# Performance work log

Hardware: AMD Instinct MI355X
Metric: run time of the kernel (lower is better)

The kernel has to match this reference:

```python
import jax, jax.numpy as jnp
import numpy as np

G = 7          # 7x7 feature map -> 49 nodes per image
N = G * G
K = 3          # knn_k
NEG_SLOPE = 0.2  # PyG GATConv default leaky_relu slope


def build_spatial_edges():
    # 8-neighborhood grid edges on the 7x7 map, directed (src -> dst)
    src, dst = [], []
    for r in range(G):
        for c in range(G):
            i = r * G + c
            for dr in (-1, 0, 1):
                for dc in (-1, 0, 1):
                    if dr == 0 and dc == 0:
                        continue
                    rr, cc = r + dr, c + dc
                    if 0 <= rr < G and 0 <= cc < G:
                        src.append(rr * G + cc)
                        dst.append(i)
    return np.array([src, dst], dtype=np.int32)

SPATIAL = build_spatial_edges()  # [2, 312]


def build_edges(x):
    """x: [B, N, F] node features -> (src, dst) each [B, E].
    Edges = spatial 8-neighborhood + feature-space kNN (k=3) + self-loops."""
    B = x.shape[0]
    sq = jnp.sum(x * x, axis=-1)                               # [B, N]
    d = sq[:, :, None] + sq[:, None, :] - 2.0 * jnp.einsum('bnf,bmf->bnm', x, x)
    d = d + jnp.eye(N, dtype=x.dtype) * 1e9                    # exclude self
    _, nbr = jax.lax.top_k(-d, K)                              # [B, N, K]
    knn_src = nbr.reshape(B, N * K)
    knn_dst = jnp.broadcast_to(jnp.repeat(jnp.arange(N, dtype=jnp.int32), K)[None], (B, N * K))
    sp = jnp.asarray(SPATIAL)
    Es = sp.shape[1]
    loops = jnp.arange(N, dtype=jnp.int32)
    src = jnp.concatenate([jnp.broadcast_to(sp[0][None], (B, Es)), knn_src.astype(jnp.int32),
                           jnp.broadcast_to(loops[None], (B, N))], axis=1)
    dst = jnp.concatenate([jnp.broadcast_to(sp[1][None], (B, Es)), knn_dst,
                           jnp.broadcast_to(loops[None], (B, N))], axis=1)
    return src, dst


def gat_layer(x, src, dst, W, a_src, a_dst, b, concat):
    """PyG-style GATConv (eval mode, no dropout). x: [N,F], src/dst: [E]."""
    H, C = a_src.shape
    h = (x @ W).reshape(N, H, C)                               # [N, H, C]
    es = jnp.sum(h * a_src[None], axis=-1)                     # [N, H]
    ed = jnp.sum(h * a_dst[None], axis=-1)                     # [N, H]
    e = jax.nn.leaky_relu(es[src] + ed[dst], NEG_SLOPE)        # [E, H]
    m = jax.ops.segment_max(e, dst, num_segments=N)            # [N, H]
    m = jnp.where(jnp.isfinite(m), m, 0.0)
    p = jnp.exp(e - m[dst])
    denom = jax.ops.segment_sum(p, dst, num_segments=N)
    alpha = p / jnp.maximum(denom[dst], 1e-16)                 # softmax over incoming edges
    out = jax.ops.segment_sum(alpha[:, :, None] * h[src], dst, num_segments=N)  # [N, H, C]
    out = out.reshape(N, H * C) if concat else out.mean(axis=1)
    return out + b


def setup_inputs() -> dict:
    key = jax.random.key(0)
    ks = jax.random.split(key, 14)
    B, F, Hd, Cd, O, NC = 256, 1024, 8, 128, 256, 14
    s = 0.05
    return {
        'feat_map': jax.random.normal(ks[0], (B, F, G, G), dtype=jnp.float32),
        'W1': jax.random.normal(ks[1], (F, Hd * Cd), dtype=jnp.float32) * s,
        'a_src1': jax.random.normal(ks[2], (Hd, Cd), dtype=jnp.float32) * s,
        'a_dst1': jax.random.normal(ks[3], (Hd, Cd), dtype=jnp.float32) * s,
        'b1': jnp.zeros((Hd * Cd,), dtype=jnp.float32),
        'W2': jax.random.normal(ks[4], (Hd * Cd, O), dtype=jnp.float32) * s,
        'a_src2': jax.random.normal(ks[5], (1, O), dtype=jnp.float32) * s,
        'a_dst2': jax.random.normal(ks[6], (1, O), dtype=jnp.float32) * s,
        'b2': jnp.zeros((O,), dtype=jnp.float32),
        'Wc1': jax.random.normal(ks[7], (O, O), dtype=jnp.float32) * s,
        'bc1': jnp.zeros((O,), dtype=jnp.float32),
        'Wc2': jax.random.normal(ks[8], (O, NC), dtype=jnp.float32) * s,
        'bc2': jnp.zeros((NC,), dtype=jnp.float32),
    }


def reference(feat_map, W1, a_src1, a_dst1, b1, W2, a_src2, a_dst2, b2, Wc1, bc1, Wc2, bc2):
    B = feat_map.shape[0]
    # backbone output relu + flatten 7x7 map into 49 nodes
    x = jax.nn.relu(feat_map).reshape(B, -1, N).transpose(0, 2, 1)  # [B, N, 1024]
    src, dst = build_edges(x)

    def per_graph(xg, sg, dg):
        h = jax.nn.elu(gat_layer(xg, sg, dg, W1, a_src1, a_dst1, b1, True))
        h = jax.nn.elu(gat_layer(h, sg, dg, W2, a_src2, a_dst2, b2, False))
        return h.mean(axis=0)                                   # global mean pool -> [256]

    pooled = jax.vmap(per_graph)(x, src, dst)                   # [B, 256]
    return jax.nn.relu(pooled @ Wc1 + bc1) @ Wc2 + bc2          # [B, 14]
```

## Files before the change

### kernel.cpp

```cpp
#include <hip/hip_runtime.h>

#define GDIM 7
#define NN 49
#define FDIM 1024
#define HD 8
#define CD 128
#define ODIM 256
#define NC 14
#define MAXE 12
#define KSPLIT 4
#define GPSTRIDE 3192

typedef __attribute__((ext_vector_type(4))) float f32x4;
typedef __attribute__((ext_vector_type(8))) short s16x8;

struct us4 { unsigned short x, y, z, w; };

__device__ __forceinline__ unsigned short f2bf(float x) {
  unsigned u = __float_as_uint(x);
  return (unsigned short)((u + 0x7fffu + ((u >> 16) & 1u)) >> 16);
}
__device__ __forceinline__ float bf2f(unsigned short h) {
  return __uint_as_float((unsigned)h << 16);
}

#define GLOAD_LDS16(g, l)                                          \
  __builtin_amdgcn_global_load_lds(                                \
      (const __attribute__((address_space(1))) void*)(g),          \
      (__attribute__((address_space(3))) void*)(l), 16, 0, 0)

__global__ void __launch_bounds__(256) relu_transpose_kernel(
    const float* __restrict__ F, float* __restrict__ X,
    unsigned short* __restrict__ Xh, unsigned short* __restrict__ Xl) {
  const int b  = blockIdx.x >> 4;
  const int f0 = (blockIdx.x & 15) << 6;
  const int tid = threadIdx.x;
  __shared__ float lds[64 * NN];
  const float* src = F + (size_t)b * FDIM * NN + (size_t)f0 * NN;
  for (int idx = tid; idx < 64 * NN; idx += 256) lds[idx] = src[idx];
  __syncthreads();
  for (int pass = 0; pass < 13; pass++) {
    int n = pass * 4 + (tid >> 6);
    int fi = tid & 63;
    if (n < NN) {
      float v = lds[fi * NN + n];
      v = v > 0.f ? v : 0.f;
      size_t o = ((size_t)b * NN + n) * FDIM + f0 + fi;
      X[o] = v;
      unsigned short h = f2bf(v);
      Xh[o] = h;
      Xl[o] = f2bf(v - bf2f(h));
    }
  }
}

__global__ void __launch_bounds__(256) knn_partial(
    const float* __restrict__ X, float* __restrict__ gramP) {
  const int gid = blockIdx.x;
  const int b = gid >> 2, p = gid & 3;
  const int tid = threadIdx.x;
  __shared__ float xs[56][68];
  const float* Xb = X + (size_t)b * NN * FDIM + p * 256;

  const int tr = tid / 14, tc = tid % 14;
  float acc[4][4];
#pragma unroll
  for (int i = 0; i < 4; i++)
#pragma unroll
    for (int j = 0; j < 4; j++) acc[i][j] = 0.f;

  for (int c0 = 0; c0 < 256; c0 += 64) {
    __syncthreads();
    for (int idx = tid; idx < NN * 16; idx += 256) {
      int n = idx >> 4, q = idx & 15;
      *(float4*)&xs[n][q << 2] =
          *(const float4*)&Xb[(size_t)n * FDIM + c0 + (q << 2)];
    }
    __syncthreads();
    if (tid < 196) {
#pragma unroll
      for (int k4 = 0; k4 < 64; k4 += 4) {
        float4 a[4], bb[4];
#pragma unroll
        for (int i = 0; i < 4; i++) a[i]  = *(const float4*)&xs[tr + 14 * i][k4];
#pragma unroll
        for (int j = 0; j < 4; j++) bb[j] = *(const float4*)&xs[tc + 14 * j][k4];
#pragma unroll
        for (int i = 0; i < 4; i++)
#pragma unroll
          for (int j = 0; j < 4; j++)
            acc[i][j] += a[i].x * bb[j].x + a[i].y * bb[j].y +
                         a[i].z * bb[j].z + a[i].w * bb[j].w;
      }
    }
  }
  if (tid < 196) {
    float* gp = gramP + (size_t)gid * GPSTRIDE;
#pragma unroll
    for (int i = 0; i < 4; i++)
#pragma unroll
      for (int j = 0; j < 4; j++)
        gp[(tr + 14 * i) * 57 + tc + 14 * j] = acc[i][j];
  }
}

__global__ void __launch_bounds__(256) knn_select(
    const float* __restrict__ gramP, int* __restrict__ knn) {
  const int b = blockIdx.x, tid = threadIdx.x;
  __shared__ float gram[NN][50];
  const float* g0 = gramP + (size_t)(b * KSPLIT) * GPSTRIDE;
  for (int idx = tid; idx < NN * NN; idx += 256) {
    int r = idx / NN, c = idx % NN;
    float s = g0[r * 57 + c] + g0[GPSTRIDE + r * 57 + c] +
              g0[2 * GPSTRIDE + r * 57 + c] + g0[3 * GPSTRIDE + r * 57 + c];
    gram[r][c] = s;
  }
  __syncthreads();
  if (tid < NN) {
    const int n = tid;
    const float sqn = gram[n][n];
    float d0 = 1e30f, d1 = 1e30f, d2 = 1e30f;
    int i0 = 0, i1 = 0, i2 = 0;
    for (int m = 0; m < NN; m++) {
      if (m == n) continue;
      float d = sqn + gram[m][m] - 2.f * gram[n][m];
      if (d < d0)      { d2=d1; i2=i1; d1=d0; i1=i0; d0=d; i0=m; }
      else if (d < d1) { d2=d1; i2=i1; d1=d;  i1=m; }
      else if (d < d2) { d2=d;  i2=m; }
    }
    knn[((size_t)b * NN + n) * 3 + 0] = i0;
    knn[((size_t)b * NN + n) * 3 + 1] = i1;
    knn[((size_t)b * NN + n) * 3 + 2] = i2;
  }
}

__global__ void __launch_bounds__(256) wconvT_kernel(
    const float* __restrict__ W, int K, int N,
    unsigned short* __restrict__ WhT, unsigned short* __restrict__ WlT) {
  __shared__ float t[64][65];
  const int nbx = N >> 6;
  const int bx = blockIdx.x % nbx, by = blockIdx.x / nbx;
  const int r0 = by << 6, c0 = bx << 6;
  const int tid = threadIdx.x;
#pragma unroll
  for (int i = 0; i < 16; i++) {
    int r = i * 4 + (tid >> 6), c = tid & 63;
    t[r][c] = W[(size_t)(r0 + r) * N + c0 + c];
  }
  __syncthreads();
#pragma unroll
  for (int i = 0; i < 16; i++) {
    int n = i * 4 + (tid >> 6);
    int k = tid & 63;
    float x = t[k][n];
    unsigned short h = f2bf(x);
    size_t o = (size_t)(c0 + n) * K + r0 + k;
    WhT[o] = h;
    WlT[o] = f2bf(x - bf2f(h));
  }
}

__global__ void __launch_bounds__(256) gemm_bf16x3(
    const unsigned short* __restrict__ A_h, const unsigned short* __restrict__ A_l,
    const unsigned short* __restrict__ BT_h, const unsigned short* __restrict__ BT_l,
    float* __restrict__ C, int M, int N, int K) {
  __shared__ unsigned short sAh[128][64], sAl[128][64];
  __shared__ unsigned short sBh[128][64], sBl[128][64];
  const int tid = threadIdx.x;
  const int w = tid >> 6, lane = tid & 63;
  const int nbx = N >> 7;
  const int nwg = gridDim.x;
  const int q = nwg >> 3, r = nwg & 7;
  const int xcd = blockIdx.x & 7, loc = blockIdx.x >> 3;
  const int wg = (xcd < r) ? (xcd * (q + 1) + loc)
                           : (r * (q + 1) + (xcd - r) * q + loc);
  const int bx = wg % nbx, by = wg / nbx;
  const int row0 = by << 7, col0 = bx << 7;
  const int wr = (w >> 1) << 6, wc = (w & 1) << 6;
  const int sgr = lane >> 3;
  const int schunk = lane & 7;
  const int fr = lane & 15;
  const int fq = lane >> 4;

  f32x4 acc[4][4];
#pragma unroll
  for (int m = 0; m < 4; m++)
#pragma unroll
    for (int n = 0; n < 4; n++) acc[m][n] = (f32x4){0.f, 0.f, 0.f, 0.f};

  for (int k0 = 0; k0 < K; k0 += 64) {
    __syncthreads();
#pragma unroll
    for (int i = 0; i < 4; i++) {
      const int rbase = (w << 5) + (i << 3);
      const int gr = rbase + sgr;
      const int sc = schunk ^ (gr & 7);
      const size_t ga = (size_t)(row0 + gr) * K + k0 + (sc << 3);
      GLOAD_LDS16(A_h + ga, &sAh[rbase][0]);
      GLOAD_LDS16(A_l + ga, &sAl[rbase][0]);
      const size_t gb = (size_t)(col0 + gr) * K + k0 + (sc << 3);
      GLOAD_LDS16(BT_h + gb, &sBh[rbase][0]);
      GLOAD_LDS16(BT_l + gb, &sBl[rbase][0]);
    }
    __syncthreads();
#pragma unroll
    for (int ks = 0; ks < 2; ks++) {
      const int cb = (ks << 2) + fq;
      s16x8 ah[4], al[4], bh[4], bl[4];
#pragma unroll
      for (int m = 0; m < 4; m++) {
        const int ra = wr + (m << 4) + fr;
        const int ca = (cb ^ (ra & 7)) << 3;
        ah[m] = *(const s16x8*)&sAh[ra][ca];
        al[m] = *(const s16x8*)&sAl[ra][ca];
        const int rb = wc + (m << 4) + fr;
        const int cbn = (cb ^ (rb & 7)) << 3;
        bh[m] = *(const s16x8*)&sBh[rb][cbn];
        bl[m] = *(const s16x8*)&sBl[rb][cbn];
      }
#pragma unroll
      for (int m = 0; m < 4; m++)
#pragma unroll
        for (int n = 0; n < 4; n++) {
          acc[m][n] = __builtin_amdgcn_mfma_f32_16x16x32_bf16(ah[m], bh[n], acc[m][n], 0, 0, 0);
          acc[m][n] = __builtin_amdgcn_mfma_f32_16x16x32_bf16(ah[m], bl[n], acc[m][n], 0, 0, 0);
          acc[m][n] = __builtin_amdgcn_mfma_f32_16x16x32_bf16(al[m], bh[n], acc[m][n], 0, 0, 0);
        }
    }
  }
  const int crow = fq << 2, ccol = fr;
#pragma unroll
  for (int m = 0; m < 4; m++)
#pragma unroll
    for (int n = 0; n < 4; n++)
#pragma unroll
      for (int v = 0; v < 4; v++)
        C[(size_t)(row0 + wr + (m << 4) + crow + v) * N + col0 + wc + (n << 4) + ccol] =
            acc[m][n][v];
}

__global__ void __launch_bounds__(256) esed1_kernel(
    const float* __restrict__ H, const float* __restrict__ a_src,
    const float* __restrict__ a_dst, float* __restrict__ es_g,
    float* __restrict__ ed_g) {
  const int n = blockIdx.x * 4 + (threadIdx.x >> 6);
  const int lane = threadIdx.x & 63;
  const int h = lane >> 3, sub = lane & 7;
  const float* hr = H + (size_t)n * FDIM + h * CD + sub * 16;
  const float* as = a_src + h * CD + sub * 16;
  const float* ad = a_dst + h * CD + sub * 16;
  float s1 = 0.f, s2 = 0.f;
#pragma unroll
  for (int c = 0; c < 16; c += 4) {
    float4 hv = *(const float4*)&hr[c];
    float4 av = *(const float4*)&as[c];
    float4 dv = *(const float4*)&ad[c];
    s1 += hv.x*av.x + hv.y*av.y + hv.z*av.z + hv.w*av.w;
    s2 += hv.x*dv.x + hv.y*dv.y + hv.z*dv.z + hv.w*dv.w;
  }
  s1 += __shfl_xor(s1, 1); s1 += __shfl_xor(s1, 2); s1 += __shfl_xor(s1, 4);
  s2 += __shfl_xor(s2, 1); s2 += __shfl_xor(s2, 2); s2 += __shfl_xor(s2, 4);
  if (sub == 0) {
    es_g[(size_t)n * HD + h] = s1;
    ed_g[(size_t)n * HD + h] = s2;
  }
}

__global__ void __launch_bounds__(256) attn1_soft(
    const float* __restrict__ es_g, const float* __restrict__ ed_g,
    const int* __restrict__ knn, int* __restrict__ srcs_g,
    int* __restrict__ cnt_g, float* __restrict__ alpha_g) {
  const int b = blockIdx.x, tid = threadIdx.x;
  __shared__ float es[NN][HD], ed[NN][HD];
  __shared__ int srcs[NN][MAXE];
  __shared__ int cnt[NN];
  for (int p = tid; p < NN * HD; p += 256) {
    es[p >> 3][p & 7] = es_g[(size_t)b * NN * HD + p];
    ed[p >> 3][p & 7] = ed_g[(size_t)b * NN * HD + p];
  }
  if (tid < NN) {
    int i = tid, r = i / GDIM, c = i % GDIM, k = 0;
    for (int dr = -1; dr <= 1; dr++)
      for (int dc = -1; dc <= 1; dc++) {
        if (dr == 0 && dc == 0) continue;
        int rr = r + dr, cc = c + dc;
        if (rr >= 0 && rr < GDIM && cc >= 0 && cc < GDIM)
          srcs[i][k++] = rr * GDIM + cc;
      }
    srcs[i][k++] = knn[((size_t)b * NN + i) * 3 + 0];
    srcs[i][k++] = knn[((size_t)b * NN + i) * 3 + 1];
    srcs[i][k++] = knn[((size_t)b * NN + i) * 3 + 2];
    srcs[i][k++] = i;
    cnt[i] = k;
    cnt_g[(size_t)b * NN + i] = k;
    for (int j = 0; j < MAXE; j++)
      srcs_g[((size_t)b * NN + i) * MAXE + j] = srcs[i][j < k ? j : 0];
  }
  __syncthreads();
  for (int p = tid; p < NN * HD; p += 256) {
    int i = p >> 3, h = p & 7;
    int k = cnt[i];
    float e[MAXE];
    float m = -1e30f;
#pragma unroll
    for (int j = 0; j < MAXE; j++) {
      if (j < k) {
        float v = es[srcs[i][j]][h] + ed[i][h];
        v = v >= 0.f ? v : 0.2f * v;
        e[j] = v;
        m = fmaxf(m, v);
      }
    }
    float denom = 0.f;
#pragma unroll
    for (int j = 0; j < MAXE; j++) {
      if (j < k) { e[j] = expf(e[j] - m); denom += e[j]; }
    }
    float inv = 1.f / fmaxf(denom, 1e-16f);
#pragma unroll
    for (int j = 0; j < MAXE; j++) {
      if (j < k)
        alpha_g[(((size_t)b * NN + i) * MAXE + j) * HD + h] = e[j] * inv;
    }
  }
}

__global__ void __launch_bounds__(256) attn1_agg(
    const float* __restrict__ H, const int* __restrict__ srcs_g,
    const int* __restrict__ cnt_g, const float* __restrict__ alpha_g,
    const float* __restrict__ b1,
    unsigned short* __restrict__ Zh, unsigned short* __restrict__ Zl) {
  const int bid = blockIdx.x;
  const int b = bid / NN;
  const int tid = threadIdx.x;
  __shared__ float al[MAXE][HD];
  __shared__ int ss[MAXE];
  const int k = cnt_g[bid];
  if (tid < MAXE * HD) al[tid >> 3][tid & 7] = alpha_g[(size_t)bid * MAXE * HD + tid];
  if (tid < MAXE) ss[tid] = srcs_g[(size_t)bid * MAXE + tid];
  __syncthreads();
  const float4* Hb = (const float4*)(H + (size_t)b * NN * FDIM);
  const int h = tid >> 5;
  float4 acc = ((const float4*)b1)[tid];
  for (int j = 0; j < k; j++) {
    float a = al[j][h];
    float4 v = Hb[(size_t)ss[j] * (FDIM / 4) + tid];
    acc.x += a * v.x; acc.y += a * v.y; acc.z += a * v.z; acc.w += a * v.w;
  }
  acc.x = acc.x > 0.f ? acc.x : expm1f(acc.x);
  acc.y = acc.y > 0.f ? acc.y : expm1f(acc.y);
  acc.z = acc.z > 0.f ? acc.z : expm1f(acc.z);
  acc.w = acc.w > 0.f ? acc.w : expm1f(acc.w);
  us4 hv, lv;
  hv.x = f2bf(acc.x); lv.x = f2bf(acc.x - bf2f(hv.x));
  hv.y = f2bf(acc.y); lv.y = f2bf(acc.y - bf2f(hv.y));
  hv.z = f2bf(acc.z); lv.z = f2bf(acc.z - bf2f(hv.z));
  hv.w = f2bf(acc.w); lv.w = f2bf(acc.w - bf2f(hv.w));
  *(us4*)&Zh[(size_t)bid * FDIM + (tid << 2)] = hv;
  *(us4*)&Zl[(size_t)bid * FDIM + (tid << 2)] = lv;
}

__global__ void __launch_bounds__(256) esed2_kernel(
    const float* __restrict__ H2, const float* __restrict__ a_src,
    const float* __restrict__ a_dst, float* __restrict__ es_g,
    float* __restrict__ ed_g) {
  const int n = blockIdx.x * 4 + (threadIdx.x >> 6);
  const int lane = threadIdx.x & 63;
  float4 hv = *(const float4*)&H2[(size_t)n * ODIM + lane * 4];
  float4 av = *(const float4*)&a_src[lane * 4];
  float4 dv = *(const float4*)&a_dst[lane * 4];
  float s1 = hv.x*av.x + hv.y*av.y + hv.z*av.z + hv.w*av.w;
  float s2 = hv.x*dv.x + hv.y*dv.y + hv.z*dv.z + hv.w*dv.w;
#pragma unroll
  for (int m = 1; m < 64; m <<= 1) {
    s1 += __shfl_xor(s1, m);
    s2 += __shfl_xor(s2, m);
  }
  if (lane == 0) { es_g[n] = s1; ed_g[n] = s2; }
}

__global__ void __launch_bounds__(256) attn2_soft(
    const float* __restrict__ es_g, const float* __restrict__ ed_g,
    const int* __restrict__ srcs_g, const int* __restrict__ cnt_g,
    float* __restrict__ alpha_g) {
  const int b = blockIdx.x, tid = threadIdx.x;
  __shared__ float es[NN], ed[NN];
  if (tid < NN) {
    es[tid] = es_g[(size_t)b * NN + tid];
    ed[tid] = ed_g[(size_t)b * NN + tid];
  }
  __syncthreads();
  if (tid < NN) {
    const int i = tid;
    const int k = cnt_g[(size_t)b * NN + i];
    float e[MAXE];
    float m = -1e30f;
#pragma unroll
    for (int j = 0; j < MAXE; j++) {
      if (j < k) {
        int s = srcs_g[((size_t)b * NN + i) * MAXE + j];
        float v = es[s] + ed[i];
        v = v >= 0.f ? v : 0.2f * v;
        e[j] = v;
        m = fmaxf(m, v);
      }
    }
    float denom = 0.f;
#pragma unroll
    for (int j = 0; j < MAXE; j++) {
      if (j < k) { e[j] = expf(e[j] - m); denom += e[j]; }
    }
    float inv = 1.f / fmaxf(denom, 1e-16f);
#pragma unroll
    for (int j = 0; j < MAXE; j++) {
      if (j < k) alpha_g[((size_t)b * NN + i) * MAXE + j] = e[j] * inv;
    }
  }
}

__global__ void __launch_bounds__(256) attn2_agg(
    const float* __restrict__ H2, const int* __restrict__ srcs_g,
    const int* __restrict__ cnt_g, const float* __restrict__ alpha_g,
    const float* __restrict__ b2, float* __restrict__ Z2) {
  const int bid = blockIdx.x;
  const int b = bid / NN;
  const int tid = threadIdx.x;
  __shared__ float al[MAXE];
  __shared__ int ss[MAXE];
  const int k = cnt_g[bid];
  if (tid < MAXE) {
    al[tid] = alpha_g[(size_t)bid * MAXE + tid];
    ss[tid] = srcs_g[(size_t)bid * MAXE + tid];
  }
  __syncthreads();
  const float* Hb = H2 + (size_t)b * NN * ODIM;
  float acc = b2[tid];
  for (int j = 0; j < k; j++)
    acc += al[j] * Hb[(size_t)ss[j] * ODIM + tid];
  acc = acc > 0.f ? acc : expm1f(acc);
  Z2[(size_t)bid * ODIM + tid] = acc;
}

__global__ void __launch_bounds__(256) classifier_kernel(
    const float* __restrict__ Z2, const float* __restrict__ Wc1,
    const float* __restrict__ bc1, const float* __restrict__ Wc2,
    const float* __restrict__ bc2, float* __restrict__ out) {
  const int b = blockIdx.x, tid = threadIdx.x;
  __shared__ float p[ODIM];
  __shared__ float t[ODIM];
  float s = 0.f;
  for (int i = 0; i < NN; i++)
    s += Z2[((size_t)b * NN + i) * ODIM + tid];
  p[tid] = s * (1.f / 49.f);
  __syncthreads();
  float a = bc1[tid];
  for (int c = 0; c < ODIM; c++) a += p[c] * Wc1[(size_t)c * ODIM + tid];
  t[tid] = a > 0.f ? a : 0.f;
  __syncthreads();
  if (tid < NC) {
    float o = bc2[tid];
    for (int j = 0; j < ODIM; j++) o += t[j] * Wc2[(size_t)j * NC + tid];
    out[(size_t)b * NC + tid] = o;
  }
}

extern "C" void kernel_launch(void* const* d_in, const int* in_sizes, int n_in,
                              void* d_out, int out_size, void* d_ws, size_t ws_size,
                              hipStream_t stream) {
  const float* feat   = (const float*)d_in[0];
  const float* W1     = (const float*)d_in[1];
  const float* a_src1 = (const float*)d_in[2];
  const float* a_dst1 = (const float*)d_in[3];
  const float* b1     = (const float*)d_in[4];
  const float* W2     = (const float*)d_in[5];
  const float* a_src2 = (const float*)d_in[6];
  const float* a_dst2 = (const float*)d_in[7];
  const float* b2     = (const float*)d_in[8];
  const float* Wc1    = (const float*)d_in[9];
  const float* bc1    = (const float*)d_in[10];
  const float* Wc2    = (const float*)d_in[11];
  const float* bc2    = (const float*)d_in[12];

  const int B = in_sizes[0] / (FDIM * NN);
  const int M = B * NN;

  const size_t xE = (size_t)M * FDIM;
  float* X  = (float*)d_ws;
  float* H1 = X + xE;
  unsigned short* Xh = (unsigned short*)(H1 + xE);
  unsigned short* Xl = Xh + xE;
  unsigned short* W1hT = Xl + xE;
  unsigned short* W1lT = W1hT + (size_t)FDIM * FDIM;
  unsigned short* W2hT = W1lT + (size_t)FDIM * FDIM;
  unsigned short* W2lT = W2hT + (size_t)ODIM * FDIM;
  int*   knn    = (int*)(W2lT + (size_t)ODIM * FDIM);
  int*   srcs_g = knn + (size_t)M * 3;
  int*   cnt_g  = srcs_g + (size_t)M * MAXE;
  float* alpha1 = (float*)(cnt_g + M);
  float* alpha2 = alpha1 + (size_t)M * MAXE * HD;
  float* gramP  = alpha2 + (size_t)M * MAXE;
  float* es1    = gramP + (size_t)B * KSPLIT * GPSTRIDE;
  float* ed1    = es1 + (size_t)M * HD;
  float* es2    = ed1 + (size_t)M * HD;
  float* ed2    = es2 + M;
  float* H2  = X;
  float* Z2  = H1;
  unsigned short* Z1h = Xh;
  unsigned short* Z1l = Xl;

  relu_transpose_kernel<<<B * 16, 256, 0, stream>>>(feat, X, Xh, Xl);
  knn_partial<<<B * KSPLIT, 256, 0, stream>>>(X, gramP);
  knn_select<<<B, 256, 0, stream>>>(gramP, knn);
  wconvT_kernel<<<(FDIM / 64) * (FDIM / 64), 256, 0, stream>>>(W1, FDIM, FDIM, W1hT, W1lT);
  wconvT_kernel<<<(FDIM / 64) * (ODIM / 64), 256, 0, stream>>>(W2, FDIM, ODIM, W2hT, W2lT);
  gemm_bf16x3<<<(M / 128) * (FDIM / 128), 256, 0, stream>>>(
      Xh, Xl, W1hT, W1lT, H1, M, FDIM, FDIM);
  esed1_kernel<<<M / 4, 256, 0, stream>>>(H1, a_src1, a_dst1, es1, ed1);
  attn1_soft<<<B, 256, 0, stream>>>(es1, ed1, knn, srcs_g, cnt_g, alpha1);
  attn1_agg<<<M, 256, 0, stream>>>(H1, srcs_g, cnt_g, alpha1, b1, Z1h, Z1l);
  gemm_bf16x3<<<(M / 128) * (ODIM / 128), 256, 0, stream>>>(
      Z1h, Z1l, W2hT, W2lT, H2, M, ODIM, FDIM);
  esed2_kernel<<<M / 4, 256, 0, stream>>>(H2, a_src2, a_dst2, es2, ed2);
  attn2_soft<<<B, 256, 0, stream>>>(es2, ed2, srcs_g, cnt_g, alpha2);
  attn2_agg<<<M, 256, 0, stream>>>(H2, srcs_g, cnt_g, alpha2, b2, Z2);
  classifier_kernel<<<B, 256, 0, stream>>>(Z2, Wc1, bc1, Wc2, bc2, (float*)d_out);
}
```

Baseline: 328.9 us.

## Fuse preprocessing kernels and compute attention scores in GEMM epilogue

Merges relu/transpose and the kNN gram partials into one launch that reads the feature map directly, so the fp32 X buffer is never written. kNN selection and both weight transposes share a second launch. The es/ed attention dot products move into the GEMM epilogue as per-64-column partial sums, which the softmax kernels add up, removing two kernels and a reread of H. The trade is extra epilogue shuffles and heavier branching in the mixed kernels; fused_pre hardcodes 4096 blocks, which assumes B=256.

```diff
diff --git a/kernel.cpp b/kernel.cpp
--- a/kernel.cpp
+++ b/kernel.cpp
@@ -29,130 +29,98 @@
       (const __attribute__((address_space(1))) void*)(g),          \
       (__attribute__((address_space(3))) void*)(l), 16, 0, 0)
 
-__global__ void __launch_bounds__(256) relu_transpose_kernel(
-    const float* __restrict__ F, float* __restrict__ X,
-    unsigned short* __restrict__ Xh, unsigned short* __restrict__ Xl) {
-  const int b  = blockIdx.x >> 4;
-  const int f0 = (blockIdx.x & 15) << 6;
+__global__ void __launch_bounds__(256) fused_pre(
+    const float* __restrict__ F, unsigned short* __restrict__ Xh,
+    unsigned short* __restrict__ Xl, float* __restrict__ gramP) {
+  __shared__ float raw[64 * 50];
+  __shared__ float xs[56][68];
   const int tid = threadIdx.x;
-  __shared__ float lds[64 * NN];
-  const float* src = F + (size_t)b * FDIM * NN + (size_t)f0 * NN;
-  for (int idx = tid; idx < 64 * NN; idx += 256) lds[idx] = src[idx];
-  __syncthreads();
-  for (int pass = 0; pass < 13; pass++) {
-    int n = pass * 4 + (tid >> 6);
-    int fi = tid & 63;
-    if (n < NN) {
-      float v = lds[fi * NN + n];
-      v = v > 0.f ? v : 0.f;
-      size_t o = ((size_t)b * NN + n) * FDIM + f0 + fi;
-      X[o] = v;
-      unsigned short h = f2bf(v);
-      Xh[o] = h;
-      Xl[o] = f2bf(v - bf2f(h));
-    }
-  }
-}
-
-__global__ void __launch_bounds__(256) knn_partial(
-    const float* __restrict__ X, float* __restrict__ gramP) {
-  const int gid = blockIdx.x;
-  const int b = gid >> 2, p = gid & 3;
-  const int tid = threadIdx.x;
-  __shared__ float xs[56][68];
-  const float* Xb = X + (size_t)b * NN * FDIM + p * 256;
-
-  const int tr = tid / 14, tc = tid % 14;
-  float acc[4][4];
-#pragma unroll
-  for (int i = 0; i < 4; i++)
-#pragma unroll
-    for (int j = 0; j < 4; j++) acc[i][j] = 0.f;
-
-  for (int c0 = 0; c0 < 256; c0 += 64) {
+  if (blockIdx.x < 4096) {
+    const int b = blockIdx.x >> 4, f0 = (blockIdx.x & 15) << 6;
+    const float* src = F + ((size_t)b * FDIM + f0) * NN;
+    for (int idx = tid; idx < 64 * NN; idx += 256) raw[idx] = src[idx];
     __syncthreads();
-    for (int idx = tid; idx < NN * 16; idx += 256) {
-      int n = idx >> 4, q = idx & 15;
-      *(float4*)&xs[n][q << 2] =
-          *(const float4*)&Xb[(size_t)n * FDIM + c0 + (q << 2)];
-    }
-    __syncthreads();
+    for (int pass = 0; pass < 13; pass++) {
+      int n = pass * 4 + (tid >> 6), fi = tid & 63;
+      if (n < NN) {
+        float v = raw[fi * NN + n];
+        v = v > 0.f ? v : 0.f;
+        size_t o = ((size_t)b * NN + n) * FDIM + f0 + fi;
+        unsigned short h = f2bf(v);
+        Xh[o] = h;
+        Xl[o] = f2bf(v - bf2f(h));
+      }
+    }
+  } else {
+    const int gid = blockIdx.x - 4096;
+    const int b = gid >> 2, p = gid & 3;
+    const int tr = tid / 14, tc = tid % 14;
+    float acc[4][4];
+#pragma unroll
+    for (int i = 0; i < 4; i++)
+#pragma unroll
+      for (int j = 0; j < 4; j++) acc[i][j] = 0.f;
+
+    for (int c0 = 0; c0 < 256; c0 += 64) {
+      const float* src = F + ((size_t)b * FDIM + p * 256 + c0) * NN;
+      __syncthreads();
+      for (int idx = tid; idx < 64 * NN; idx += 256) {
+        float v = src[idx];
+        raw[idx] = v > 0.f ? v : 0.f;
+      }
+      __syncthreads();
+      for (int idx = tid; idx < 64 * NN; idx += 256) {
+        int cc = idx & 63, n = idx >> 6;
+        xs[n][cc] = raw[cc * NN + n];
+      }
+      __syncthreads();
+      if (tid < 196) {
+#pragma unroll
+        for (int k4 = 0; k4 < 64; k4 += 4) {
+          float4 a[4], bb[4];
+#pragma unroll
+          for (int i = 0; i < 4; i++) a[i]  = *(const float4*)&xs[tr + 14 * i][k4];
+#pragma unroll
+          for (int j = 0; j < 4; j++) bb[j] = *(const float4*)&xs[tc + 14 * j][k4];
+#pragma unroll
+          for (int i = 0; i < 4; i++)
+#pragma unroll
+            for (int j = 0; j < 4; j++)
+              acc[i][j] += a[i].x * bb[j].x + a[i].y * bb[j].y +
+                           a[i].z * bb[j].z + a[i].w * bb[j].w;
+        }
+      }
+    }
     if (tid < 196) {
-#pragma unroll
-      for (int k4 = 0; k4 < 64; k4 += 4) {
-        float4 a[4], bb[4];
-#pragma unroll
-        for (int i = 0; i < 4; i++) a[i]  = *(const float4*)&xs[tr + 14 * i][k4];
-#pragma unroll
-        for (int j = 0; j < 4; j++) bb[j] = *(const float4*)&xs[tc + 14 * j][k4];
-#pragma unroll
-        for (int i = 0; i < 4; i++)
-#pragma unroll
-          for (int j = 0; j < 4; j++)
-            acc[i][j] += a[i].x * bb[j].x + a[i].y * bb[j].y +
-                         a[i].z * bb[j].z + a[i].w * bb[j].w;
-      }
-    }
-  }
-  if (tid < 196) {
-    float* gp = gramP + (size_t)gid * GPSTRIDE;
-#pragma unroll
-    for (int i = 0; i < 4; i++)
-#pragma unroll
-      for (int j = 0; j < 4; j++)
-        gp[(tr + 14 * i) * 57 + tc + 14 * j] = acc[i][j];
-  }
-}
-
-__global__ void __launch_bounds__(256) knn_select(
-    const float* __restrict__ gramP, int* __restrict__ knn) {
-  const int b = blockIdx.x, tid = threadIdx.x;
-  __shared__ float gram[NN][50];
-  const float* g0 = gramP + (size_t)(b * KSPLIT) * GPSTRIDE;
-  for (int idx = tid; idx < NN * NN; idx += 256) {
-    int r = idx / NN, c = idx % NN;
-    float s = g0[r * 57 + c] + g0[GPSTRIDE + r * 57 + c] +
-              g0[2 * GPSTRIDE + r * 57 + c] + g0[3 * GPSTRIDE + r * 57 + c];
-    gram[r][c] = s;
-  }
-  __syncthreads();
-  if (tid < NN) {
-    const int n = tid;
-    const float sqn = gram[n][n];
-    float d0 = 1e30f, d1 = 1e30f, d2 = 1e30f;
-    int i0 = 0, i1 = 0, i2 = 0;
-    for (int m = 0; m < NN; m++) {
-      if (m == n) continue;
-      float d = sqn + gram[m][m] - 2.f * gram[n][m];
-      if (d < d0)      { d2=d1; i2=i1; d1=d0; i1=i0; d0=d; i0=m; }
-      else if (d < d1) { d2=d1; i2=i1; d1=d;  i1=m; }
-      else if (d < d2) { d2=d;  i2=m; }
-    }
-    knn[((size_t)b * NN + n) * 3 + 0] = i0;
-    knn[((size_t)b * NN + n) * 3 + 1] = i1;
-    knn[((size_t)b * NN + n) * 3 + 2] = i2;
-  }
-}
-
-__global__ void __launch_bounds__(256) wconvT_kernel(
-    const float* __restrict__ W, int K, int N,
-    unsigned short* __restrict__ WhT, unsigned short* __restrict__ WlT) {
-  __shared__ float t[64][65];
+      float* gp = gramP + (size_t)gid * GPSTRIDE;
+#pragma unroll
+      for (int i = 0; i < 4; i++)
+#pragma unroll
+        for (int j = 0; j < 4; j++)
+          gp[(tr + 14 * i) * 57 + tc + 14 * j] = acc[i][j];
+    }
+  }
+}
+
+__device__ void wconvT_body(const float* __restrict__ W, int K, int N,
+                            unsigned short* __restrict__ WhT,
+                            unsigned short* __restrict__ WlT, int blk,
+                            float* t ) {
   const int nbx = N >> 6;
-  const int bx = blockIdx.x % nbx, by = blockIdx.x / nbx;
+  const int bx = blk % nbx, by = blk / nbx;
   const int r0 = by << 6, c0 = bx << 6;
   const int tid = threadIdx.x;
 #pragma unroll
   for (int i = 0; i < 16; i++) {
     int r = i * 4 + (tid >> 6), c = tid & 63;
-    t[r][c] = W[(size_t)(r0 + r) * N + c0 + c];
+    t[r * 65 + c] = W[(size_t)(r0 + r) * N + c0 + c];
   }
   __syncthreads();
 #pragma unroll
   for (int i = 0; i < 16; i++) {
     int n = i * 4 + (tid >> 6);
     int k = tid & 63;
-    float x = t[k][n];
+    float x = t[k * 65 + n];
     unsigned short h = f2bf(x);
     size_t o = (size_t)(c0 + n) * K + r0 + k;
     WhT[o] = h;
@@ -160,10 +128,53 @@
   }
 }
 
+__global__ void __launch_bounds__(256) misc_kernel(
+    const float* __restrict__ gramP, int* __restrict__ knn,
+    const float* __restrict__ W1, unsigned short* __restrict__ W1hT,
+    unsigned short* __restrict__ W1lT, const float* __restrict__ W2,
+    unsigned short* __restrict__ W2hT, unsigned short* __restrict__ W2lT) {
+  __shared__ float shbuf[64 * 65];
+  const int tid = threadIdx.x;
+  if (blockIdx.x < 256) {
+    const int b = blockIdx.x;
+    float* gram = shbuf;
+    const float* g0 = gramP + (size_t)(b * KSPLIT) * GPSTRIDE;
+    for (int idx = tid; idx < NN * NN; idx += 256) {
+      int r = idx / NN, c = idx % NN;
+      gram[r * 50 + c] = g0[r * 57 + c] + g0[GPSTRIDE + r * 57 + c] +
+                         g0[2 * GPSTRIDE + r * 57 + c] +
+                         g0[3 * GPSTRIDE + r * 57 + c];
+    }
+    __syncthreads();
+    if (tid < NN) {
+      const int n = tid;
+      const float sqn = gram[n * 50 + n];
+      float d0 = 1e30f, d1 = 1e30f, d2 = 1e30f;
+      int i0 = 0, i1 = 0, i2 = 0;
+      for (int m = 0; m < NN; m++) {
+        if (m == n) continue;
+        float d = sqn + gram[m * 50 + m] - 2.f * gram[n * 50 + m];
+        if (d < d0)      { d2=d1; i2=i1; d1=d0; i1=i0; d0=d; i0=m; }
+        else if (d < d1) { d2=d1; i2=i1; d1=d;  i1=m; }
+        else if (d < d2) { d2=d;  i2=m; }
+      }
+      knn[((size_t)b * NN + n) * 3 + 0] = i0;
+      knn[((size_t)b * NN + n) * 3 + 1] = i1;
+      knn[((size_t)b * NN + n) * 3 + 2] = i2;
+    }
+  } else if (blockIdx.x < 512) {
+    wconvT_body(W1, FDIM, FDIM, W1hT, W1lT, blockIdx.x - 256, shbuf);
+  } else {
+    wconvT_body(W2, FDIM, ODIM, W2hT, W2lT, blockIdx.x - 512, shbuf);
+  }
+}
+
 __global__ void __launch_bounds__(256) gemm_bf16x3(
     const unsigned short* __restrict__ A_h, const unsigned short* __restrict__ A_l,
     const unsigned short* __restrict__ BT_h, const unsigned short* __restrict__ BT_l,
-    float* __restrict__ C, int M, int N, int K) {
+    float* __restrict__ C, int M, int N, int K,
+    const float* __restrict__ av, const float* __restrict__ dv,
+    float* __restrict__ esp, float* __restrict__ edp) {
   __shared__ unsigned short sAh[128][64], sAl[128][64];
   __shared__ unsigned short sBh[128][64], sBl[128][64];
   const int tid = threadIdx.x;
@@ -237,37 +248,38 @@
       for (int v = 0; v < 4; v++)
         C[(size_t)(row0 + wr + (m << 4) + crow + v) * N + col0 + wc + (n << 4) + ccol] =
             acc[m][n][v];
-}
-
-__global__ void __launch_bounds__(256) esed1_kernel(
-    const float* __restrict__ H, const float* __restrict__ a_src,
-    const float* __restrict__ a_dst, float* __restrict__ es_g,
-    float* __restrict__ ed_g) {
-  const int n = blockIdx.x * 4 + (threadIdx.x >> 6);
-  const int lane = threadIdx.x & 63;
-  const int h = lane >> 3, sub = lane & 7;
-  const float* hr = H + (size_t)n * FDIM + h * CD + sub * 16;
-  const float* as = a_src + h * CD + sub * 16;
-  const float* ad = a_dst + h * CD + sub * 16;
-  float s1 = 0.f, s2 = 0.f;
-#pragma unroll
-  for (int c = 0; c < 16; c += 4) {
-    float4 hv = *(const float4*)&hr[c];
-    float4 av = *(const float4*)&as[c];
-    float4 dv = *(const float4*)&ad[c];
-    s1 += hv.x*av.x + hv.y*av.y + hv.z*av.z + hv.w*av.w;
-    s2 += hv.x*dv.x + hv.y*dv.y + hv.z*dv.z + hv.w*dv.w;
-  }
-  s1 += __shfl_xor(s1, 1); s1 += __shfl_xor(s1, 2); s1 += __shfl_xor(s1, 4);
-  s2 += __shfl_xor(s2, 1); s2 += __shfl_xor(s2, 2); s2 += __shfl_xor(s2, 4);
-  if (sub == 0) {
-    es_g[(size_t)n * HD + h] = s1;
-    ed_g[(size_t)n * HD + h] = s2;
-  }
+
+  const int pstride = N >> 6;
+  const int part = (col0 + wc) >> 6;
+  float asv[4], adv[4];
+#pragma unroll
+  for (int n = 0; n < 4; n++) {
+    int cidx = col0 + wc + (n << 4) + fr;
+    asv[n] = av[cidx];
+    adv[n] = dv[cidx];
+  }
+#pragma unroll
+  for (int m = 0; m < 4; m++)
+#pragma unroll
+    for (int v = 0; v < 4; v++) {
+      float s = acc[m][0][v] * asv[0] + acc[m][1][v] * asv[1] +
+                acc[m][2][v] * asv[2] + acc[m][3][v] * asv[3];
+      float d = acc[m][0][v] * adv[0] + acc[m][1][v] * adv[1] +
+                acc[m][2][v] * adv[2] + acc[m][3][v] * adv[3];
+      s += __shfl_xor(s, 1); s += __shfl_xor(s, 2);
+      s += __shfl_xor(s, 4); s += __shfl_xor(s, 8);
+      d += __shfl_xor(d, 1); d += __shfl_xor(d, 2);
+      d += __shfl_xor(d, 4); d += __shfl_xor(d, 8);
+      if (fr == 0) {
+        int row = row0 + wr + (m << 4) + (fq << 2) + v;
+        esp[(size_t)row * pstride + part] = s;
+        edp[(size_t)row * pstride + part] = d;
+      }
+    }
 }
 
 __global__ void __launch_bounds__(256) attn1_soft(
-    const float* __restrict__ es_g, const float* __restrict__ ed_g,
+    const float* __restrict__ es1p, const float* __restrict__ ed1p,
     const int* __restrict__ knn, int* __restrict__ srcs_g,
     int* __restrict__ cnt_g, float* __restrict__ alpha_g) {
   const int b = blockIdx.x, tid = threadIdx.x;
@@ -275,8 +287,10 @@
   __shared__ int srcs[NN][MAXE];
   __shared__ int cnt[NN];
   for (int p = tid; p < NN * HD; p += 256) {
-    es[p >> 3][p & 7] = es_g[(size_t)b * NN * HD + p];
-    ed[p >> 3][p & 7] = ed_g[(size_t)b * NN * HD + p];
+    int n = p >> 3, h = p & 7;
+    size_t base = ((size_t)(b * NN + n)) * 16 + h * 2;
+    es[n][h] = es1p[base] + es1p[base + 1];
+    ed[n][h] = ed1p[base] + ed1p[base + 1];
   }
   if (tid < NN) {
     int i = tid, r = i / GDIM, c = i % GDIM, k = 0;
@@ -360,34 +374,16 @@
   *(us4*)&Zl[(size_t)bid * FDIM + (tid << 2)] = lv;
 }
 
-__global__ void __launch_bounds__(256) esed2_kernel(
-    const float* __restrict__ H2, const float* __restrict__ a_src,
-    const float* __restrict__ a_dst, float* __restrict__ es_g,
-    float* __restrict__ ed_g) {
-  const int n = blockIdx.x * 4 + (threadIdx.x >> 6);
-  const int lane = threadIdx.x & 63;
-  float4 hv = *(const float4*)&H2[(size_t)n * ODIM + lane * 4];
-  float4 av = *(const float4*)&a_src[lane * 4];
-  float4 dv = *(const float4*)&a_dst[lane * 4];
-  float s1 = hv.x*av.x + hv.y*av.y + hv.z*av.z + hv.w*av.w;
-  float s2 = hv.x*dv.x + hv.y*dv.y + hv.z*dv.z + hv.w*dv.w;
-#pragma unroll
-  for (int m = 1; m < 64; m <<= 1) {
-    s1 += __shfl_xor(s1, m);
-    s2 += __shfl_xor(s2, m);
-  }
-  if (lane == 0) { es_g[n] = s1; ed_g[n] = s2; }
-}
-
 __global__ void __launch_bounds__(256) attn2_soft(
-    const float* __restrict__ es_g, const float* __restrict__ ed_g,
+    const float* __restrict__ es2p, const float* __restrict__ ed2p,
     const int* __restrict__ srcs_g, const int* __restrict__ cnt_g,
     float* __restrict__ alpha_g) {
   const int b = blockIdx.x, tid = threadIdx.x;
   __shared__ float es[NN], ed[NN];
   if (tid < NN) {
-    es[tid] = es_g[(size_t)b * NN + tid];
-    ed[tid] = ed_g[(size_t)b * NN + tid];
+    size_t base = ((size_t)(b * NN + tid)) * 4;
+    es[tid] = es2p[base] + es2p[base + 1] + es2p[base + 2] + es2p[base + 3];
+    ed[tid] = ed2p[base] + ed2p[base + 1] + ed2p[base + 2] + ed2p[base + 3];
   }
   __syncthreads();
   if (tid < NN) {
@@ -485,8 +481,7 @@
   const int M = B * NN;
 
   const size_t xE = (size_t)M * FDIM;
-  float* X  = (float*)d_ws;
-  float* H1 = X + xE;
+  float* H1 = (float*)d_ws;
   unsigned short* Xh = (unsigned short*)(H1 + xE);
   unsigned short* Xl = Xh + xE;
   unsigned short* W1hT = Xl + xE;
@@ -499,29 +494,24 @@
   float* alpha1 = (float*)(cnt_g + M);
   float* alpha2 = alpha1 + (size_t)M * MAXE * HD;
   float* gramP  = alpha2 + (size_t)M * MAXE;
-  float* es1    = gramP + (size_t)B * KSPLIT * GPSTRIDE;
-  float* ed1    = es1 + (size_t)M * HD;
-  float* es2    = ed1 + (size_t)M * HD;
-  float* ed2    = es2 + M;
-  float* H2  = X;
-  float* Z2  = H1;
+  float* es1p   = gramP + (size_t)B * KSPLIT * GPSTRIDE;
+  float* ed1p   = es1p + (size_t)M * 16;
+  float* es2p   = ed1p + (size_t)M * 16;
+  float* ed2p   = es2p + (size_t)M * 4;
+  float* H2  = H1;
+  float* Z2  = H1 + (size_t)M * ODIM;
   unsigned short* Z1h = Xh;
   unsigned short* Z1l = Xl;
 
-  relu_transpose_kernel<<<B * 16, 256, 0, stream>>>(feat, X, Xh, Xl);
-  knn_partial<<<B * KSPLIT, 256, 0, stream>>>(X, gramP);
-  knn_select<<<B, 256, 0, stream>>>(gramP, knn);
-  wconvT_kernel<<<(FDIM / 64) * (FDIM / 64), 256, 0, stream>>>(W1, FDIM, FDIM, W1hT, W1lT);
-  wconvT_kernel<<<(FDIM / 64) * (ODIM / 64), 256, 0, stream>>>(W2, FDIM, ODIM, W2hT, W2lT);
+  fused_pre<<<B * 16 + B * KSPLIT, 256, 0, stream>>>(feat, Xh, Xl, gramP);
+  misc_kernel<<<576, 256, 0, stream>>>(gramP, knn, W1, W1hT, W1lT, W2, W2hT, W2lT);
   gemm_bf16x3<<<(M / 128) * (FDIM / 128), 256, 0, stream>>>(
-      Xh, Xl, W1hT, W1lT, H1, M, FDIM, FDIM);
-  esed1_kernel<<<M / 4, 256, 0, stream>>>(H1, a_src1, a_dst1, es1, ed1);
-  attn1_soft<<<B, 256, 0, stream>>>(es1, ed1, knn, srcs_g, cnt_g, alpha1);
+      Xh, Xl, W1hT, W1lT, H1, M, FDIM, FDIM, a_src1, a_dst1, es1p, ed1p);
+  attn1_soft<<<B, 256, 0, stream>>>(es1p, ed1p, knn, srcs_g, cnt_g, alpha1);
   attn1_agg<<<M, 256, 0, stream>>>(H1, srcs_g, cnt_g, alpha1, b1, Z1h, Z1l);
   gemm_bf16x3<<<(M / 128) * (ODIM / 128), 256, 0, stream>>>(
-      Z1h, Z1l, W2hT, W2lT, H2, M, ODIM, FDIM);
-  esed2_kernel<<<M / 4, 256, 0, stream>>>(H2, a_src2, a_dst2, es2, ed2);
-  attn2_soft<<<B, 256, 0, stream>>>(es2, ed2, srcs_g, cnt_g, alpha2);
+      Z1h, Z1l, W2hT, W2lT, H2, M, ODIM, FDIM, a_src2, a_dst2, es2p, ed2p);
+  attn2_soft<<<B, 256, 0, stream>>>(es2p, ed2p, srcs_g, cnt_g, alpha2);
   attn2_agg<<<M, 256, 0, stream>>>(H2, srcs_g, cnt_g, alpha2, b2, Z2);
   classifier_kernel<<<B, 256, 0, stream>>>(Z2, Wc1, bc1, Wc2, bc2, (float*)d_out);
 }
```

New measurement: 396.6 us. 1.21x slower.
